# Performance work log

Hardware: AMD Instinct MI355X
Metric: run time of the kernel (lower is better)

The kernel has to match this reference:

```python
import jax, jax.numpy as jnp
import numpy as np

B, N, T, DIN, DOUT, H = 8, 512, 128, 128, 128, 8
HD = DOUT // H  # head_dim


def setup_inputs() -> dict:
    key = jax.random.key(0)
    ks = jax.random.split(key, 9)
    h = jax.random.normal(ks[0], (B, N, T, DIN), dtype=jnp.float32)
    adj = jax.random.uniform(ks[1], (B, T, N, 1), dtype=jnp.float32)
    mask = jax.random.randint(ks[2], (B, N, T, 1), 0, 2).astype(jnp.float32)
    s1 = 1.0 / np.sqrt(DIN)
    W1 = jax.random.uniform(ks[3], (DIN, DOUT), jnp.float32, -s1, s1)
    b1 = jax.random.uniform(ks[4], (DOUT,), jnp.float32, -s1, s1)
    sa = 1.0 / np.sqrt(2 * HD)
    Wa = jax.random.uniform(ks[5], (2 * HD, 1), jnp.float32, -sa, sa)
    ba = jax.random.uniform(ks[6], (1,), jnp.float32, -sa, sa)
    s2 = 1.0 / np.sqrt(2 * DOUT)
    W2 = jax.random.uniform(ks[7], (2 * DOUT, DOUT), jnp.float32, -s2, s2)
    b2 = jax.random.uniform(ks[8], (DOUT,), jnp.float32, -s2, s2)
    return {"h": h, "adj": adj, "mask": mask, "W1": W1, "b1": b1,
            "Wa": Wa, "ba": ba, "W2": W2, "b2": b2}


def reference(h, adj, mask, W1, b1, Wa, ba, W2, b2):
    # h: (B,N,T,DIN) -> project to (B,N,T,DOUT)
    hp = jnp.einsum('bntd,de->bnte', h, W1) + b1
    target_h = hp[:, 0]                      # (B,T,DOUT)
    # (B,T,H,N,HD)
    hh = hp.reshape(B, N, T, H, HD).transpose(0, 2, 3, 1, 4)
    # Original builds an NxNx2HD concat then a Linear and keeps only src-row 0.
    # Equivalent additive decomposition: score = h0.Wsrc + hj.Wdst + b.
    Wsrc, Wdst = Wa[:HD, 0], Wa[HD:, 0]
    s0 = jnp.einsum('bthd,d->bth', hh[:, :, :, 0], Wsrc)   # (B,T,H)
    sj = jnp.einsum('bthnd,d->bthn', hh, Wdst)             # (B,T,H,N)
    score = s0[..., None] + sj + ba[0]                     # (B,T,H,N)
    # mask: (B,N,T,1) -> (B,T,1,N), broadcast over heads
    m = mask[:, :, :, 0].transpose(0, 2, 1)[:, :, None, :]
    # adj: (B,T,N,1) -> (B,T,1,N)
    a = adj[:, :, :, 0][:, :, None, :]
    a = jnp.where(a == 0, 1e9, a)
    a = jnp.where(m > 0, 1.0 / a, a)
    score = jnp.where(m == 0, -1e9, score)
    attn = jax.nn.softmax(score, axis=-1) * a              # (B,T,H,N)
    agg = jnp.einsum('bthn,bthnd->bthd', attn, hh).reshape(B, T, DOUT)
    out = jnp.concatenate([agg, target_h], axis=-1) @ W2 + b2
    return out
```

## Files before the change

kernel.cpp:

```cpp
#include <hip/hip_runtime.h>

#define NN   512
#define TT   128
#define DD   128
#define NC   64
#define NCHUNK 8
#define SR   132
#define WR   68

__global__ void gat_prep(const float* __restrict__ W1, const float* __restrict__ b1,
                         const float* __restrict__ Wa, const float* __restrict__ ba,
                         float* __restrict__ ws)
{
  int idx = blockIdx.x*256 + threadIdx.x;
  int d = idx >> 3, h = idx & 7;
  float v = 0.f, u = 0.f;
  for (int j = 0; j < 16; ++j){
    float w1 = W1[d*DD + h*16 + j];
    v += w1 * Wa[16 + j];
    u += w1 * Wa[j];
  }
  ws[(h>>1)*256 + (d>>2)*8 + (h&1)*4 + (d&3)] = v;
  ws[2048 + d*8 + h] = u;
  if (idx < 8){
    float ec = ba[0];
    for (int j = 0; j < 16; ++j)
      ec += b1[idx*16 + j] * (Wa[j] + Wa[16 + j]);
    ws[3072 + idx] = ec;
  }
}

__global__ __launch_bounds__(256, 4) void gat_main(
    const float* __restrict__ hin, const float* __restrict__ adj, const float* __restrict__ mask,
    const float* __restrict__ W1,  const float* __restrict__ b1,
    const float* __restrict__ W2,  const float* __restrict__ b2,
    const float* __restrict__ ws,  float* __restrict__ out)
{
  __shared__ __align__(16) float hchd[NC*SR];
  __shared__ __align__(16) float wTt[8*WR];
  __shared__ float Karr[8], RL[8];
  __shared__ float targ[128];

  float* const aggfin = hchd;
  float* const catbuf = hchd + 8*SR;
  float* const oppart = hchd + 8*SR + 256;

  const int t    = threadIdx.x;
  const int bb   = blockIdx.x >> 7;
  const int tt   = blockIdx.x & 127;
  const int wave = t >> 6;
  const int lane = t & 63;
  const int h0   = 2*wave;

  const int wv = __builtin_amdgcn_readfirstlane(wave);
  const float4* __restrict__ vg = (const float4*)(ws + (wv << 8));

  const int dq = lane & 31;
  const int rh = lane >> 5;

  float mrun0 = -1e30f, mrun1 = -1e30f;
  float Zp0 = 0.f, Zp1 = 0.f, SWp0 = 0.f, SWp1 = 0.f;
  float acc0 = 0.f, acc1 = 0.f, acc2 = 0.f, acc3 = 0.f;
  float acc4 = 0.f, acc5 = 0.f, acc6 = 0.f, acc7 = 0.f;

  const float4* __restrict__ hg4 = (const float4*)hin;
  const long dI = 8L*TT*(DD/4);
  const long dC = (long)NC*TT*(DD/4);
  const long g0 = ((long)(bb*NN + (t>>5))*TT + tt)*(DD/4) + (t & 31);
  const int  l0 = (t>>5)*SR + 4*(t & 31);

  float4 pf[8];
  #pragma unroll
  for (int i = 0; i < 8; ++i) pf[i] = hg4[g0 + (long)i*dI];
  #pragma unroll
  for (int i = 0; i < 8; ++i) *(float4*)&hchd[l0 + i*(8*SR)] = pf[i];
  __syncthreads();

  if (t < 128){
    float a = b1[t];
    for (int d = 0; d < 128; ++d)
      a += hchd[d] * W1[d*DD + t];
    targ[t] = a;
  } else if (t < 136){
    int h8 = t - 128;
    float a = ws[3072 + h8];
    for (int d = 0; d < 128; ++d)
      a += hchd[d] * ws[2048 + d*8 + h8];
    Karr[h8] = a;
  }
  __syncthreads();

  const float K0 = Karr[h0], K1 = Karr[h0 + 1];

  for (int c = 0; c < NCHUNK; ++c){
    const int ng = c*NC + lane;
    const float mv = mask[(long)(bb*NN + ng)*TT + tt];
    const float av = adj[(long)(bb*TT + tt)*NN + ng];

    if (c < NCHUNK-1){
      const long gc = g0 + (long)(c+1)*dC;
      #pragma unroll
      for (int i = 0; i < 8; ++i) pf[i] = hg4[gc + (long)i*dI];
    }

    float s0 = K0, s1 = K1;
    {
      const float4* rowp = (const float4*)&hchd[lane*SR];
      #pragma unroll 8
      for (int j = 0; j < 32; ++j){
        float4 r4 = rowp[j];
        float4 va = vg[2*j], vb = vg[2*j + 1];
        s0 += r4.x*va.x + r4.y*va.y + r4.z*va.z + r4.w*va.w;
        s1 += r4.x*vb.x + r4.y*vb.y + r4.z*vb.z + r4.w*vb.w;
      }
    }
    const float inva = (av == 0.f) ? 1e-9f : (1.f/av);

    float sm0 = (mv > 0.f) ? s0 : -1e30f;
    float sm1 = (mv > 0.f) ? s1 : -1e30f;
    #pragma unroll
    for (int off = 32; off >= 1; off >>= 1){
      sm0 = fmaxf(sm0, __shfl_xor(sm0, off));
      sm1 = fmaxf(sm1, __shfl_xor(sm1, off));
    }
    float mn0 = fmaxf(mrun0, sm0), mn1 = fmaxf(mrun1, sm1);
    float sc0 = __expf(mrun0 - mn0), sc1 = __expf(mrun1 - mn1);
    mrun0 = mn0; mrun1 = mn1;

    float e0 = (mv > 0.f) ? __expf(s0 - mn0) : 0.f;
    float e1 = (mv > 0.f) ? __expf(s1 - mn1) : 0.f;
    float w0 = e0*inva, w1 = e1*inva;
    wTt[h0*WR + lane]       = w0;
    wTt[(h0 + 1)*WR + lane] = w1;
    Zp0  = Zp0*sc0  + e0;  Zp1  = Zp1*sc1  + e1;
    SWp0 = SWp0*sc0 + w0;  SWp1 = SWp1*sc1 + w1;

    {
      acc0 *= sc0; acc1 *= sc0; acc2 *= sc0; acc3 *= sc0;
      acc4 *= sc1; acc5 *= sc1; acc6 *= sc1; acc7 *= sc1;
      const int rbase = rh*32;
      const float* wr0 = &wTt[h0*WR + rbase];
      const float* wr1 = &wTt[(h0 + 1)*WR + rbase];
      const float* hb  = &hchd[rbase*SR + 4*dq];
      #pragma unroll 4
      for (int g = 0; g < 8; ++g){
        float4 wa = *(const float4*)&wr0[4*g];
        float4 wb = *(const float4*)&wr1[4*g];
        float4 r0 = *(const float4*)&hb[(4*g + 0)*SR];
        float4 r1 = *(const float4*)&hb[(4*g + 1)*SR];
        float4 r2 = *(const float4*)&hb[(4*g + 2)*SR];
        float4 r3 = *(const float4*)&hb[(4*g + 3)*SR];
        acc0 += wa.x*r0.x + wa.y*r1.x + wa.z*r2.x + wa.w*r3.x;
        acc1 += wa.x*r0.y + wa.y*r1.y + wa.z*r2.y + wa.w*r3.y;
        acc2 += wa.x*r0.z + wa.y*r1.z + wa.z*r2.z + wa.w*r3.z;
        acc3 += wa.x*r0.w + wa.y*r1.w + wa.z*r2.w + wa.w*r3.w;
        acc4 += wb.x*r0.x + wb.y*r1.x + wb.z*r2.x + wb.w*r3.x;
        acc5 += wb.x*r0.y + wb.y*r1.y + wb.z*r2.y + wb.w*r3.y;
        acc6 += wb.x*r0.z + wb.y*r1.z + wb.z*r2.z + wb.w*r3.z;
        acc7 += wb.x*r0.w + wb.y*r1.w + wb.z*r2.w + wb.w*r3.w;
      }
    }
    __syncthreads();
    if (c < NCHUNK-1){
      #pragma unroll
      for (int i = 0; i < 8; ++i) *(float4*)&hchd[l0 + i*(8*SR)] = pf[i];
      __syncthreads();
    }
  }

  #pragma unroll
  for (int off = 32; off >= 1; off >>= 1){
    Zp0  += __shfl_xor(Zp0,  off);  Zp1  += __shfl_xor(Zp1,  off);
    SWp0 += __shfl_xor(SWp0, off);  SWp1 += __shfl_xor(SWp1, off);
  }
  acc0 += __shfl_xor(acc0, 32); acc1 += __shfl_xor(acc1, 32);
  acc2 += __shfl_xor(acc2, 32); acc3 += __shfl_xor(acc3, 32);
  acc4 += __shfl_xor(acc4, 32); acc5 += __shfl_xor(acc5, 32);
  acc6 += __shfl_xor(acc6, 32); acc7 += __shfl_xor(acc7, 32);

  if (lane == 0){
    RL[h0]     = SWp0 / Zp0;
    RL[h0 + 1] = SWp1 / Zp1;
  }
  {
    float invZ = (rh == 0) ? (1.f/Zp0) : (1.f/Zp1);
    float4 o;
    o.x = ((rh == 0) ? acc0 : acc4) * invZ;
    o.y = ((rh == 0) ? acc1 : acc5) * invZ;
    o.z = ((rh == 0) ? acc2 : acc6) * invZ;
    o.w = ((rh == 0) ? acc3 : acc7) * invZ;
    *(float4*)&aggfin[(h0 + rh)*SR + 4*dq] = o;
  }
  __syncthreads();

  if (t < 128){
    int h2 = t >> 4;
    float a = RL[h2] * b1[t];
    for (int d = 0; d < 128; ++d)
      a += aggfin[h2*SR + d] * W1[d*DD + t];
    catbuf[t]       = a;
    catbuf[128 + t] = targ[t];
  }
  __syncthreads();

  {
    int j = t & 127, kh = t >> 7;
    float o = 0.f;
    for (int k = kh*128; k < kh*128 + 128; ++k)
      o += catbuf[k] * W2[k*DD + j];
    oppart[t] = o;
  }
  __syncthreads();
  if (t < 128)
    out[(long)blockIdx.x*128 + t] = oppart[t] + oppart[128 + t] + b2[t];
}

extern "C" void kernel_launch(void* const* d_in, const int* in_sizes, int n_in,
                              void* d_out, int out_size, void* d_ws, size_t ws_size,
                              hipStream_t stream) {
  const float* h    = (const float*)d_in[0];
  const float* adj  = (const float*)d_in[1];
  const float* mask = (const float*)d_in[2];
  const float* W1   = (const float*)d_in[3];
  const float* b1   = (const float*)d_in[4];
  const float* Wa   = (const float*)d_in[5];
  const float* ba   = (const float*)d_in[6];
  const float* W2   = (const float*)d_in[7];
  const float* b2   = (const float*)d_in[8];
  float* ws  = (float*)d_ws;
  float* out = (float*)d_out;

  gat_prep<<<4, 256, 0, stream>>>(W1, b1, Wa, ba, ws);
  gat_main<<<1024, 256, 0, stream>>>(h, adj, mask, W1, b1, W2, b2, ws, out);
}
```

Before: 434.6 us.

## Double-buffer fp16 LDS tiles and prefetch two chunks ahead with new aggregation mapping

Stores the per-chunk h tile in shared memory as fp16 in two alternating buffers, so global loads for chunk c+2 and the LDS store for chunk c+1 overlap with compute on chunk c, removing one barrier per chunk. The mask and adj values are also prefetched one chunk ahead. The aggregation is remapped so each lane handles 8 columns across 16 rows, with a cross-lane reduction at the end. The fp16 storage halves LDS footprint and traffic but introduces rounding error in both the scores and the aggregated features.

```diff
diff --git a/kernel.cpp b/kernel.cpp
--- a/kernel.cpp
+++ b/kernel.cpp
@@ -1,11 +1,12 @@
 #include <hip/hip_runtime.h>
+#include <hip/hip_fp16.h>
 
 #define NN   512
 #define TT   128
 #define DD   128
 #define NC   64
 #define NCHUNK 8
-#define SR   132
+#define SRH  136
 #define WR   68
 
 __global__ void gat_prep(const float* __restrict__ W1, const float* __restrict__ b1,
@@ -30,20 +31,37 @@
   }
 }
 
+static __device__ __forceinline__ float2 up2(unsigned u){
+  union { unsigned u; __half2 h; } c; c.u = u;
+  return __half22float2(c.h);
+}
+static __device__ __forceinline__ unsigned pk2(float x, float y){
+  union { __half2 h; unsigned u; } c;
+  c.h = __float22half2_rn(make_float2(x, y));
+  return c.u;
+}
+static __device__ __forceinline__ void st8(ushort* p, float4 a, float4 b){
+  uint4 u;
+  u.x = pk2(a.x, a.y); u.y = pk2(a.z, a.w);
+  u.z = pk2(b.x, b.y); u.w = pk2(b.z, b.w);
+  *(uint4*)p = u;
+}
+
 __global__ __launch_bounds__(256, 4) void gat_main(
     const float* __restrict__ hin, const float* __restrict__ adj, const float* __restrict__ mask,
     const float* __restrict__ W1,  const float* __restrict__ b1,
     const float* __restrict__ W2,  const float* __restrict__ b2,
     const float* __restrict__ ws,  float* __restrict__ out)
 {
-  __shared__ __align__(16) float hchd[NC*SR];
+  __shared__ __align__(16) ushort tile0[NC*SRH];
+  __shared__ __align__(16) ushort tile1[NC*SRH];
   __shared__ __align__(16) float wTt[8*WR];
   __shared__ float Karr[8], RL[8];
   __shared__ float targ[128];
 
-  float* const aggfin = hchd;
-  float* const catbuf = hchd + 8*SR;
-  float* const oppart = hchd + 8*SR + 256;
+  float* const aggfin = (float*)tile0;
+  float* const catbuf = (float*)tile0 + 1056;
+  float* const oppart = (float*)tile0 + 1312;
 
   const int t    = threadIdx.x;
   const int bb   = blockIdx.x >> 7;
@@ -55,37 +73,50 @@
   const int wv = __builtin_amdgcn_readfirstlane(wave);
   const float4* __restrict__ vg = (const float4*)(ws + (wv << 8));
 
-  const int dq = lane & 31;
-  const int rh = lane >> 5;
+  const int o = lane & 15;
+  const int q = lane >> 4;
 
   float mrun0 = -1e30f, mrun1 = -1e30f;
   float Zp0 = 0.f, Zp1 = 0.f, SWp0 = 0.f, SWp1 = 0.f;
-  float acc0 = 0.f, acc1 = 0.f, acc2 = 0.f, acc3 = 0.f;
-  float acc4 = 0.f, acc5 = 0.f, acc6 = 0.f, acc7 = 0.f;
-
+  float4 aA0 = {0,0,0,0}, aA1 = {0,0,0,0};
+  float4 aB0 = {0,0,0,0}, aB1 = {0,0,0,0};
+
+  const int rw = t >> 4, co = t & 15;
   const float4* __restrict__ hg4 = (const float4*)hin;
-  const long dI = 8L*TT*(DD/4);
-  const long dC = (long)NC*TT*(DD/4);
-  const long g0 = ((long)(bb*NN + (t>>5))*TT + tt)*(DD/4) + (t & 31);
-  const int  l0 = (t>>5)*SR + 4*(t & 31);
-
-  float4 pf[8];
-  #pragma unroll
-  for (int i = 0; i < 8; ++i) pf[i] = hg4[g0 + (long)i*dI];
-  #pragma unroll
-  for (int i = 0; i < 8; ++i) *(float4*)&hchd[l0 + i*(8*SR)] = pf[i];
+  const long dI4 = 16L*TT*(DD/4);
+  const long dC4 = (long)NC*TT*(DD/4);
+  const long g0f4 = ((long)(bb*NN + rw)*TT + tt)*(DD/4) + 2*co;
+
+  float4 pfa0, pfb0, pfa1, pfb1, pfa2, pfb2, pfa3, pfb3;
+
+#define PF_LOAD(C) do{ const long _g = g0f4 + (long)(C)*dC4; \
+    pfa0 = hg4[_g];          pfb0 = hg4[_g + 1]; \
+    pfa1 = hg4[_g +   dI4];  pfb1 = hg4[_g +   dI4 + 1]; \
+    pfa2 = hg4[_g + 2*dI4];  pfb2 = hg4[_g + 2*dI4 + 1]; \
+    pfa3 = hg4[_g + 3*dI4];  pfb3 = hg4[_g + 3*dI4 + 1]; }while(0)
+#define PF_STORE(TB) do{ \
+    st8(&(TB)[(rw +  0)*SRH + 8*co], pfa0, pfb0); \
+    st8(&(TB)[(rw + 16)*SRH + 8*co], pfa1, pfb1); \
+    st8(&(TB)[(rw + 32)*SRH + 8*co], pfa2, pfb2); \
+    st8(&(TB)[(rw + 48)*SRH + 8*co], pfa3, pfb3); }while(0)
+
+  PF_LOAD(0);
+  float mvc = mask[(long)(bb*NN + lane)*TT + tt];
+  float avc = adj[(long)(bb*TT + tt)*NN + lane];
+  PF_STORE(tile0);
+  PF_LOAD(1);
   __syncthreads();
 
   if (t < 128){
     float a = b1[t];
     for (int d = 0; d < 128; ++d)
-      a += hchd[d] * W1[d*DD + t];
+      a += __half2float(((const __half*)tile0)[d]) * W1[d*DD + t];
     targ[t] = a;
   } else if (t < 136){
     int h8 = t - 128;
     float a = ws[3072 + h8];
     for (int d = 0; d < 128; ++d)
-      a += hchd[d] * ws[2048 + d*8 + h8];
+      a += __half2float(((const __half*)tile0)[d]) * ws[2048 + d*8 + h8];
     Karr[h8] = a;
   }
   __syncthreads();
@@ -93,31 +124,35 @@
   const float K0 = Karr[h0], K1 = Karr[h0 + 1];
 
   for (int c = 0; c < NCHUNK; ++c){
-    const int ng = c*NC + lane;
-    const float mv = mask[(long)(bb*NN + ng)*TT + tt];
-    const float av = adj[(long)(bb*TT + tt)*NN + ng];
-
+    ushort* tb = (c & 1) ? tile1 : tile0;
+    ushort* to = (c & 1) ? tile0 : tile1;
+
+    if (c < NCHUNK-1) PF_STORE(to);
+    if (c < NCHUNK-2) PF_LOAD(c+2);
+    float mvn = 0.f, avn = 0.f;
     if (c < NCHUNK-1){
-      const long gc = g0 + (long)(c+1)*dC;
-      #pragma unroll
-      for (int i = 0; i < 8; ++i) pf[i] = hg4[gc + (long)i*dI];
+      mvn = mask[(long)(bb*NN + (c+1)*NC + lane)*TT + tt];
+      avn = adj[(long)(bb*TT + tt)*NN + (c+1)*NC + lane];
     }
 
     float s0 = K0, s1 = K1;
     {
-      const float4* rowp = (const float4*)&hchd[lane*SR];
-      #pragma unroll 8
-      for (int j = 0; j < 32; ++j){
-        float4 r4 = rowp[j];
-        float4 va = vg[2*j], vb = vg[2*j + 1];
-        s0 += r4.x*va.x + r4.y*va.y + r4.z*va.z + r4.w*va.w;
-        s1 += r4.x*vb.x + r4.y*vb.y + r4.z*vb.z + r4.w*vb.w;
+      const ushort* rowp = &tb[lane*SRH];
+      #pragma unroll 4
+      for (int j = 0; j < 16; ++j){
+        uint4 u = *(const uint4*)&rowp[8*j];
+        float2 p0 = up2(u.x), p1 = up2(u.y), p2 = up2(u.z), p3 = up2(u.w);
+        float4 va0 = vg[4*j], vb0 = vg[4*j+1], va1 = vg[4*j+2], vb1 = vg[4*j+3];
+        s0 += p0.x*va0.x + p0.y*va0.y + p1.x*va0.z + p1.y*va0.w
+            + p2.x*va1.x + p2.y*va1.y + p3.x*va1.z + p3.y*va1.w;
+        s1 += p0.x*vb0.x + p0.y*vb0.y + p1.x*vb0.z + p1.y*vb0.w
+            + p2.x*vb1.x + p2.y*vb1.y + p3.x*vb1.z + p3.y*vb1.w;
       }
     }
-    const float inva = (av == 0.f) ? 1e-9f : (1.f/av);
-
-    float sm0 = (mv > 0.f) ? s0 : -1e30f;
-    float sm1 = (mv > 0.f) ? s1 : -1e30f;
+    const float inva = (avc == 0.f) ? 1e-9f : (1.f/avc);
+
+    float sm0 = (mvc > 0.f) ? s0 : -1e30f;
+    float sm1 = (mvc > 0.f) ? s1 : -1e30f;
     #pragma unroll
     for (int off = 32; off >= 1; off >>= 1){
       sm0 = fmaxf(sm0, __shfl_xor(sm0, off));
@@ -127,8 +162,8 @@
     float sc0 = __expf(mrun0 - mn0), sc1 = __expf(mrun1 - mn1);
     mrun0 = mn0; mrun1 = mn1;
 
-    float e0 = (mv > 0.f) ? __expf(s0 - mn0) : 0.f;
-    float e1 = (mv > 0.f) ? __expf(s1 - mn1) : 0.f;
+    float e0 = (mvc > 0.f) ? __expf(s0 - mn0) : 0.f;
+    float e1 = (mvc > 0.f) ? __expf(s1 - mn1) : 0.f;
     float w0 = e0*inva, w1 = e1*inva;
     wTt[h0*WR + lane]       = w0;
     wTt[(h0 + 1)*WR + lane] = w1;
@@ -136,60 +171,61 @@
     SWp0 = SWp0*sc0 + w0;  SWp1 = SWp1*sc1 + w1;
 
     {
-      acc0 *= sc0; acc1 *= sc0; acc2 *= sc0; acc3 *= sc0;
-      acc4 *= sc1; acc5 *= sc1; acc6 *= sc1; acc7 *= sc1;
-      const int rbase = rh*32;
-      const float* wr0 = &wTt[h0*WR + rbase];
-      const float* wr1 = &wTt[(h0 + 1)*WR + rbase];
-      const float* hb  = &hchd[rbase*SR + 4*dq];
-      #pragma unroll 4
-      for (int g = 0; g < 8; ++g){
-        float4 wa = *(const float4*)&wr0[4*g];
-        float4 wb = *(const float4*)&wr1[4*g];
-        float4 r0 = *(const float4*)&hb[(4*g + 0)*SR];
-        float4 r1 = *(const float4*)&hb[(4*g + 1)*SR];
-        float4 r2 = *(const float4*)&hb[(4*g + 2)*SR];
-        float4 r3 = *(const float4*)&hb[(4*g + 3)*SR];
-        acc0 += wa.x*r0.x + wa.y*r1.x + wa.z*r2.x + wa.w*r3.x;
-        acc1 += wa.x*r0.y + wa.y*r1.y + wa.z*r2.y + wa.w*r3.y;
-        acc2 += wa.x*r0.z + wa.y*r1.z + wa.z*r2.z + wa.w*r3.z;
-        acc3 += wa.x*r0.w + wa.y*r1.w + wa.z*r2.w + wa.w*r3.w;
-        acc4 += wb.x*r0.x + wb.y*r1.x + wb.z*r2.x + wb.w*r3.x;
-        acc5 += wb.x*r0.y + wb.y*r1.y + wb.z*r2.y + wb.w*r3.y;
-        acc6 += wb.x*r0.z + wb.y*r1.z + wb.z*r2.z + wb.w*r3.z;
-        acc7 += wb.x*r0.w + wb.y*r1.w + wb.z*r2.w + wb.w*r3.w;
+      aA0.x*=sc0; aA0.y*=sc0; aA0.z*=sc0; aA0.w*=sc0;
+      aA1.x*=sc0; aA1.y*=sc0; aA1.z*=sc0; aA1.w*=sc0;
+      aB0.x*=sc1; aB0.y*=sc1; aB0.z*=sc1; aB0.w*=sc1;
+      aB1.x*=sc1; aB1.y*=sc1; aB1.z*=sc1; aB1.w*=sc1;
+#define AGGROW(R, WA, WB) { \
+      uint4 u = *(const uint4*)&tb[(R)*SRH + 8*o]; \
+      float2 p0 = up2(u.x), p1 = up2(u.y), p2 = up2(u.z), p3 = up2(u.w); \
+      aA0.x += (WA)*p0.x; aA0.y += (WA)*p0.y; aA0.z += (WA)*p1.x; aA0.w += (WA)*p1.y; \
+      aA1.x += (WA)*p2.x; aA1.y += (WA)*p2.y; aA1.z += (WA)*p3.x; aA1.w += (WA)*p3.y; \
+      aB0.x += (WB)*p0.x; aB0.y += (WB)*p0.y; aB0.z += (WB)*p1.x; aB0.w += (WB)*p1.y; \
+      aB1.x += (WB)*p2.x; aB1.y += (WB)*p2.y; aB1.z += (WB)*p3.x; aB1.w += (WB)*p3.y; }
+      #pragma unroll
+      for (int k = 0; k < 4; ++k){
+        float4 wA = *(const float4*)&wTt[h0*WR + 16*q + 4*k];
+        float4 wB = *(const float4*)&wTt[(h0+1)*WR + 16*q + 4*k];
+        const int rb = 16*q + 4*k;
+        AGGROW(rb+0, wA.x, wB.x);
+        AGGROW(rb+1, wA.y, wB.y);
+        AGGROW(rb+2, wA.z, wB.z);
+        AGGROW(rb+3, wA.w, wB.w);
       }
     }
     __syncthreads();
-    if (c < NCHUNK-1){
-      #pragma unroll
-      for (int i = 0; i < 8; ++i) *(float4*)&hchd[l0 + i*(8*SR)] = pf[i];
-      __syncthreads();
-    }
-  }
-
+    mvc = mvn; avc = avn;
+  }
+
+#define R2X(v) { v += __shfl_xor(v, 16); v += __shfl_xor(v, 32); }
+  R2X(aA0.x) R2X(aA0.y) R2X(aA0.z) R2X(aA0.w)
+  R2X(aA1.x) R2X(aA1.y) R2X(aA1.z) R2X(aA1.w)
+  R2X(aB0.x) R2X(aB0.y) R2X(aB0.z) R2X(aB0.w)
+  R2X(aB1.x) R2X(aB1.y) R2X(aB1.z) R2X(aB1.w)
   #pragma unroll
   for (int off = 32; off >= 1; off >>= 1){
     Zp0  += __shfl_xor(Zp0,  off);  Zp1  += __shfl_xor(Zp1,  off);
     SWp0 += __shfl_xor(SWp0, off);  SWp1 += __shfl_xor(SWp1, off);
   }
-  acc0 += __shfl_xor(acc0, 32); acc1 += __shfl_xor(acc1, 32);
-  acc2 += __shfl_xor(acc2, 32); acc3 += __shfl_xor(acc3, 32);
-  acc4 += __shfl_xor(acc4, 32); acc5 += __shfl_xor(acc5, 32);
-  acc6 += __shfl_xor(acc6, 32); acc7 += __shfl_xor(acc7, 32);
-
   if (lane == 0){
     RL[h0]     = SWp0 / Zp0;
     RL[h0 + 1] = SWp1 / Zp1;
   }
   {
-    float invZ = (rh == 0) ? (1.f/Zp0) : (1.f/Zp1);
-    float4 o;
-    o.x = ((rh == 0) ? acc0 : acc4) * invZ;
-    o.y = ((rh == 0) ? acc1 : acc5) * invZ;
-    o.z = ((rh == 0) ? acc2 : acc6) * invZ;
-    o.w = ((rh == 0) ? acc3 : acc7) * invZ;
-    *(float4*)&aggfin[(h0 + rh)*SR + 4*dq] = o;
+    const float invZ0 = 1.f/Zp0, invZ1 = 1.f/Zp1;
+    if (q == 0){
+      float4 v0 = aA0, v1 = aA1;
+      v0.x*=invZ0; v0.y*=invZ0; v0.z*=invZ0; v0.w*=invZ0;
+      v1.x*=invZ0; v1.y*=invZ0; v1.z*=invZ0; v1.w*=invZ0;
+      *(float4*)&aggfin[h0*132 + 8*o]     = v0;
+      *(float4*)&aggfin[h0*132 + 8*o + 4] = v1;
+    } else if (q == 1){
+      float4 v0 = aB0, v1 = aB1;
+      v0.x*=invZ1; v0.y*=invZ1; v0.z*=invZ1; v0.w*=invZ1;
+      v1.x*=invZ1; v1.y*=invZ1; v1.z*=invZ1; v1.w*=invZ1;
+      *(float4*)&aggfin[(h0+1)*132 + 8*o]     = v0;
+      *(float4*)&aggfin[(h0+1)*132 + 8*o + 4] = v1;
+    }
   }
   __syncthreads();
 
@@ -197,7 +233,7 @@
     int h2 = t >> 4;
     float a = RL[h2] * b1[t];
     for (int d = 0; d < 128; ++d)
-      a += aggfin[h2*SR + d] * W1[d*DD + t];
+      a += aggfin[h2*132 + d] * W1[d*DD + t];
     catbuf[t]       = a;
     catbuf[128 + t] = targ[t];
   }
@@ -205,10 +241,10 @@
 
   {
     int j = t & 127, kh = t >> 7;
-    float o = 0.f;
+    float o2 = 0.f;
     for (int k = kh*128; k < kh*128 + 128; ++k)
-      o += catbuf[k] * W2[k*DD + j];
-    oppart[t] = o;
+      o2 += catbuf[k] * W2[k*DD + j];
+    oppart[t] = o2;
   }
   __syncthreads();
   if (t < 128)
```

New measurement: 467.6 us. +7.6%, slower.
